# Performance work log

Measured on AMD Instinct MI355X. Metric: run time of the kernel, lower is better.

## Reference

```python
import jax, jax.numpy as jnp
import numpy as np

DIM = 1024
HEADS = 16
HEAD_DIM = 64
INNER = HEADS * HEAD_DIM  # 1024
SCALE = 8.0
LN_EPS = 1e-5
NORM_EPS = 1e-12  # F.normalize default eps


def layer_norm(x, g, b):
    m = jnp.mean(x, axis=-1, keepdims=True)
    v = jnp.mean((x - m) ** 2, axis=-1, keepdims=True)
    return (x - m) * jax.lax.rsqrt(v + LN_EPS) * g + b


def l2_normalize(x):
    n = jnp.sqrt(jnp.sum(x * x, axis=-1, keepdims=True))
    return x / jnp.maximum(n, NORM_EPS)


def setup_inputs() -> dict:
    key = jax.random.key(0)
    ks = jax.random.split(key, 8)
    B, N, T = 4, 4096, 256
    s = 0.02
    return {
        "x": jax.random.normal(ks[0], (B, N, DIM), jnp.float32),
        "context": jax.random.normal(ks[1], (B, T, DIM), jnp.float32),
        "Wq": jax.random.normal(ks[2], (DIM, INNER), jnp.float32) * s,
        "Wkv": jax.random.normal(ks[3], (DIM, 2 * INNER), jnp.float32) * s,
        "Wo": jax.random.normal(ks[4], (INNER, DIM), jnp.float32) * s,
        "null_kv": jax.random.normal(ks[5], (2, HEAD_DIM), jnp.float32),
        "q_scale": jnp.ones((HEAD_DIM,), jnp.float32),
        "k_scale": jnp.ones((HEAD_DIM,), jnp.float32),
        "ln_in_g": jnp.ones((DIM,), jnp.float32),
        "ln_in_b": jnp.zeros((DIM,), jnp.float32),
        "ln_ctx_g": jnp.ones((DIM,), jnp.float32),
        "ln_ctx_b": jnp.zeros((DIM,), jnp.float32),
        "ln_out_g": jnp.ones((DIM,), jnp.float32),
        "ln_out_b": jnp.zeros((DIM,), jnp.float32),
    }


def reference(x, context, Wq, Wkv, Wo, null_kv, q_scale, k_scale,
              ln_in_g, ln_in_b, ln_ctx_g, ln_ctx_b, ln_out_g, ln_out_b):
    B, N, _ = x.shape
    T = context.shape[1]
    xn = layer_norm(x, ln_in_g, ln_in_b)
    cn = layer_norm(context, ln_ctx_g, ln_ctx_b)
    q = xn @ Wq                      # [B, N, INNER]
    kv = cn @ Wkv                    # [B, T, 2*INNER]
    k, v = jnp.split(kv, 2, axis=-1)
    # split heads: b s (h d) -> b h s d
    def split_heads(t):
        b, s, _ = t.shape
        return t.reshape(b, s, HEADS, HEAD_DIM).transpose(0, 2, 1, 3)
    q, k, v = split_heads(q), split_heads(k), split_heads(v)
    # null kv token appended along kv-seq dim
    nk = jnp.broadcast_to(null_kv[0], (B, HEADS, 1, HEAD_DIM))
    nv = jnp.broadcast_to(null_kv[1], (B, HEADS, 1, HEAD_DIM))
    k = jnp.concatenate([k, nk], axis=2)   # [B, H, T+1, D]
    v = jnp.concatenate([v, nv], axis=2)
    q = l2_normalize(q) * q_scale
    k = l2_normalize(k) * k_scale
    scores = jnp.einsum('bhid,bhkd->bhik', q, k) * SCALE
    attn = jax.nn.softmax(scores, axis=-1)
    out = jnp.einsum('bhik,bhkd->bhid', attn, v)   # [B, H, N, D]
    out = out.transpose(0, 2, 1, 3).reshape(B, N, INNER)
    out = out @ Wo
    return layer_norm(out, ln_out_g, ln_out_b)
```

## Files before the change

kernel.cpp:

```cpp
#include <hip/hip_runtime.h>
#include <cstdint>
#include <cstddef>

typedef _Float16 f16;
typedef _Float16 f16x4 __attribute__((ext_vector_type(4)));
typedef _Float16 f16x8 __attribute__((ext_vector_type(8)));
typedef float f32x4 __attribute__((ext_vector_type(4)));

#define DIM 1024
#define B_ 4
#define N_ 4096
#define TKP 288
#define SCALE_ 8.0f
#define LOG2E 1.4426950408889634f

__device__ __forceinline__ void gload_lds16(const void* g, void* l) {
  __builtin_amdgcn_global_load_lds(
      reinterpret_cast<const __attribute__((address_space(1))) uint32_t*>(
          reinterpret_cast<uintptr_t>(g)),
      reinterpret_cast<__attribute__((address_space(3))) uint32_t*>(
          reinterpret_cast<uintptr_t>(l)),
      16, 0, 0);
}

__global__ void transpose_w_kernel(const float* __restrict__ W, f16* __restrict__ WT,
                                   int K, int N) {
  __shared__ float tile[32][33];
  int nt = N >> 5;
  int tk = blockIdx.x / nt, tn = blockIdx.x % nt;
  int tx = threadIdx.x & 31, ty = threadIdx.x >> 5;
#pragma unroll
  for (int p = 0; p < 32; p += 8)
    tile[ty + p][tx] = W[(size_t)(tk * 32 + ty + p) * N + tn * 32 + tx];
  __syncthreads();
#pragma unroll
  for (int p = 0; p < 32; p += 8)
    WT[(size_t)(tn * 32 + ty + p) * K + tk * 32 + tx] = (f16)tile[tx][ty + p];
}

template <typename OUT_T>
__global__ void ln_kernel(const float* __restrict__ in, const float* __restrict__ g,
                          const float* __restrict__ bb, OUT_T* __restrict__ out) {
  int row = blockIdx.x;
  int t = threadIdx.x;
  const float4* rp = (const float4*)(in + (size_t)row * DIM);
  float4 v = rp[t];
  float s = v.x + v.y + v.z + v.w;
  float ss = v.x * v.x + v.y * v.y + v.z * v.z + v.w * v.w;
#pragma unroll
  for (int m = 1; m < 64; m <<= 1) { s += __shfl_xor(s, m); ss += __shfl_xor(ss, m); }
  __shared__ float red[8];
  int w = t >> 6;
  if ((t & 63) == 0) { red[w * 2] = s; red[w * 2 + 1] = ss; }
  __syncthreads();
  s = red[0] + red[2] + red[4] + red[6];
  ss = red[1] + red[3] + red[5] + red[7];
  float mean = s * (1.0f / DIM);
  float var = ss * (1.0f / DIM) - mean * mean;
  float rstd = rsqrtf(var + 1e-5f);
  float4 gv = ((const float4*)g)[t];
  float4 bv = ((const float4*)bb)[t];
  float o0 = (v.x - mean) * rstd * gv.x + bv.x;
  float o1 = (v.y - mean) * rstd * gv.y + bv.y;
  float o2 = (v.z - mean) * rstd * gv.z + bv.z;
  float o3 = (v.w - mean) * rstd * gv.w + bv.w;
  if constexpr (sizeof(OUT_T) == 2) {
    f16x4 h = {(f16)o0, (f16)o1, (f16)o2, (f16)o3};
    *(f16x4*)((f16*)out + (size_t)row * DIM + t * 4) = h;
  } else {
    float4 o = {o0, o1, o2, o3};
    *(float4*)((float*)out + (size_t)row * DIM + t * 4) = o;
  }
}

template <bool OUT_F32>
__global__ __launch_bounds__(256, 2) void gemm_nt_kernel(
    const f16* __restrict__ A, const f16* __restrict__ Bt, void* __restrict__ C,
    int M, int N, int K) {
  __shared__ f16 As[128 * 64];
  __shared__ f16 Bs[128 * 64];
  int nb = N >> 7;
  int cpx = gridDim.x >> 3;
  int wg = ((int)blockIdx.x & 7) * cpx + ((int)blockIdx.x >> 3);
  int bm = wg / nb, bn = wg % nb;
  int t = threadIdx.x;
  int lane = t & 63, w = t >> 6;
  int wm = w >> 1, wn = w & 1;
  int r16 = lane & 15, g4 = lane >> 4;
  f32x4 acc[4][4] = {};
  for (int k0 = 0; k0 < K; k0 += 64) {
#pragma unroll
    for (int i = 0; i < 4; ++i) {
      int li = i * 256 + t;
      int r = li >> 3, c = li & 7;
      int kc = ((c ^ (r & 7)) << 3);
      gload_lds16(A + (size_t)(bm * 128 + r) * K + k0 + kc, (char*)As + li * 16);
      gload_lds16(Bt + (size_t)(bn * 128 + r) * K + k0 + kc, (char*)Bs + li * 16);
    }
    asm volatile("s_waitcnt vmcnt(0)" ::: "memory");
    __syncthreads();
#pragma unroll
    for (int ks = 0; ks < 2; ++ks) {
      f16x8 af[4], bf[4];
#pragma unroll
      for (int mi = 0; mi < 4; ++mi) {
        int r = wm * 64 + mi * 16 + r16;
        int cidx = ks * 4 + g4;
        af[mi] = *(const f16x8*)(As + r * 64 + ((cidx ^ (r & 7)) << 3));
      }
#pragma unroll
      for (int ni = 0; ni < 4; ++ni) {
        int r = wn * 64 + ni * 16 + r16;
        int cidx = ks * 4 + g4;
        bf[ni] = *(const f16x8*)(Bs + r * 64 + ((cidx ^ (r & 7)) << 3));
      }
#pragma unroll
      for (int mi = 0; mi < 4; ++mi)
#pragma unroll
        for (int ni = 0; ni < 4; ++ni)
          acc[mi][ni] = __builtin_amdgcn_mfma_f32_16x16x32_f16(af[mi], bf[ni],
                                                               acc[mi][ni], 0, 0, 0);
    }
    __syncthreads();
  }
  int cr0 = bm * 128 + wm * 64;
  int cc = bn * 128 + wn * 64 + r16;
#pragma unroll
  for (int mi = 0; mi < 4; ++mi)
#pragma unroll
    for (int ni = 0; ni < 4; ++ni)
#pragma unroll
      for (int j = 0; j < 4; ++j) {
        int row = cr0 + mi * 16 + g4 * 4 + j;
        int col = cc + ni * 16;
        if constexpr (OUT_F32)
          ((float*)C)[(size_t)row * N + col] = acc[mi][ni][j];
        else
          ((f16*)C)[(size_t)row * N + col] = (f16)acc[mi][ni][j];
      }
}

__global__ void prep_kv_kernel(const f16* __restrict__ kv, const float* __restrict__ nullkv,
                               const float* __restrict__ ks, f16* __restrict__ Karr,
                               f16* __restrict__ Varr) {
  int bh = blockIdx.x;
  int b = bh >> 4, h = bh & 15;
  int t = threadIdx.x;
  __shared__ f16 vt[256][65];
  const f16* krow = kv + (size_t)(b * 256 + t) * 2048 + h * 64;
  const f16* vrow = krow + 1024;
  f16x8 kd[8];
  float ss = 0.0f;
#pragma unroll
  for (int i = 0; i < 8; ++i) {
    kd[i] = *(const f16x8*)(krow + i * 8);
#pragma unroll
    for (int j = 0; j < 8; ++j) { float x = (float)kd[i][j]; ss += x * x; }
  }
  float inv = 1.0f / fmaxf(sqrtf(ss), 1e-12f);
  f16* kout = Karr + ((size_t)bh * TKP + t) * 64;
#pragma unroll
  for (int i = 0; i < 8; ++i) {
    f16x8 o;
#pragma unroll
    for (int j = 0; j < 8; ++j) o[j] = (f16)((float)kd[i][j] * inv * ks[i * 8 + j]);
    *(f16x8*)(kout + i * 8) = o;
  }
#pragma unroll
  for (int i = 0; i < 8; ++i) {
    f16x8 vv = *(const f16x8*)(vrow + i * 8);
#pragma unroll
    for (int j = 0; j < 8; ++j) vt[t][i * 8 + j] = vv[j];
  }
  if (t < 32) {
    f16* kr = Karr + ((size_t)bh * TKP + 256 + t) * 64;
    if (t == 0) {
      float ssn = 0.0f;
      for (int d = 0; d < 64; ++d) ssn += nullkv[d] * nullkv[d];
      float invn = 1.0f / fmaxf(sqrtf(ssn), 1e-12f);
      for (int d = 0; d < 64; ++d) kr[d] = (f16)(nullkv[d] * invn * ks[d]);
    } else {
      for (int d = 0; d < 64; ++d) kr[d] = (f16)0.0f;
    }
  }
  __syncthreads();
  f16* vbase = Varr + (size_t)bh * 64 * TKP;
  int pcol = (t & ~31) | (((t & 15) << 1) | ((t >> 4) & 1));
  for (int d = 0; d < 64; ++d) vbase[(size_t)d * TKP + pcol] = vt[t][d];
#pragma unroll
  for (int i = 0; i < 8; ++i) {
    int idx = i * 256 + t;
    int d = idx >> 5, key = 256 + (idx & 31);
    vbase[(size_t)d * TKP + key] = (key == 256) ? (f16)nullkv[64 + d] : (f16)0.0f;
  }
}

__global__ __launch_bounds__(256, 4) void attn_kernel(
    const f16* __restrict__ Q, const f16* __restrict__ Karr,
    const f16* __restrict__ Varr, const float* __restrict__ qs,
    const float* __restrict__ ksc, f16* __restrict__ O) {
  int wgid = ((int)blockIdx.x & 7) * 256 + ((int)blockIdx.x >> 3);
  int qb = wgid & 31, bh = wgid >> 5;
  int b = bh >> 4, h = bh & 15;
  int t = threadIdx.x, lane = t & 63, w = t >> 6;
  int r16 = lane & 15, g4 = lane >> 4;
  int row0 = b * N_ + qb * 128 + w * 32;
  int col0 = h * 64;
  const f16* Kp = Karr + (size_t)bh * TKP * 64;
  const f16* Vp = Varr + (size_t)bh * 64 * TKP;
  __shared__ f16 Plds[4][32 * 40];
  f16* Pw = &Plds[w][0];
  float mq = fabsf(qs[lane]), mk = fabsf(ksc[lane]);
#pragma unroll
  for (int m = 1; m < 64; m <<= 1) {
    mq = fmaxf(mq, __shfl_xor(mq, m));
    mk = fmaxf(mk, __shfl_xor(mk, m));
  }
  const float c1 = SCALE_ * LOG2E;
  const float c2 = SCALE_ * mq * mk * LOG2E;
  float qsv[2][8];
#pragma unroll
  for (int kdh = 0; kdh < 2; ++kdh)
#pragma unroll
    for (int i = 0; i < 8; ++i) qsv[kdh][i] = qs[kdh * 32 + g4 * 8 + i];
  f16x8 qf[2][2];
#pragma unroll
  for (int mi = 0; mi < 2; ++mi) {
    float f[2][8];
    float ssq = 0.0f;
#pragma unroll
    for (int kdh = 0; kdh < 2; ++kdh) {
      f16x8 v = *(const f16x8*)(Q + (size_t)(row0 + mi * 16 + r16) * DIM +
                                col0 + kdh * 32 + g4 * 8);
#pragma unroll
      for (int i = 0; i < 8; ++i) { f[kdh][i] = (float)v[i]; ssq += f[kdh][i] * f[kdh][i]; }
    }
    ssq += __shfl_xor(ssq, 16);
    ssq += __shfl_xor(ssq, 32);
    float inv = 1.0f / fmaxf(sqrtf(ssq), 1e-12f);
#pragma unroll
    for (int kdh = 0; kdh < 2; ++kdh) {
      f16x8 o;
#pragma unroll
      for (int i = 0; i < 8; ++i) o[i] = (f16)(f[kdh][i] * inv * qsv[kdh][i]);
      qf[mi][kdh] = o;
    }
  }
  f32x4 o[2][4] = {};
  float part[2][4] = {};
  for (int kt = 0; kt < 9; ++kt) {
    int key0 = kt * 32;
    f16x8 kf[2][2];
#pragma unroll
    for (int ni = 0; ni < 2; ++ni)
#pragma unroll
      for (int kdh = 0; kdh < 2; ++kdh)
        kf[ni][kdh] = *(const f16x8*)(Kp + (size_t)(key0 + ni * 16 + r16) * 64 +
                                      kdh * 32 + g4 * 8);
    f32x4 s[2][2] = {};
    __builtin_amdgcn_s_setprio(1);
#pragma unroll
    for (int kdh = 0; kdh < 2; ++kdh)
#pragma unroll
      for (int mi = 0; mi < 2; ++mi)
#pragma unroll
        for (int ni = 0; ni < 2; ++ni)
          s[mi][ni] = __builtin_amdgcn_mfma_f32_16x16x32_f16(qf[mi][kdh], kf[ni][kdh],
                                                             s[mi][ni], 0, 0, 0);
    __builtin_amdgcn_s_setprio(0);
    bool va = (key0 + r16 <= 256), vb = (key0 + 16 + r16 <= 256);
#pragma unroll
    for (int mi = 0; mi < 2; ++mi) {
#pragma unroll
      for (int j = 0; j < 4; ++j) {
        float p0 = exp2f(s[mi][0][j] * c1 - c2);
        float p1 = exp2f(s[mi][1][j] * c1 - c2);
        p0 = va ? p0 : 0.0f;
        p1 = vb ? p1 : 0.0f;
        part[mi][j] += p0 + p1;
        int prow = mi * 16 + g4 * 4 + j;
        auto pk = __builtin_amdgcn_cvt_pkrtz(p0, p1);
        ((uint32_t*)(Pw + prow * 40))[r16] = __builtin_bit_cast(uint32_t, pk);
      }
    }
    f16x8 vf[4];
#pragma unroll
    for (int nd = 0; nd < 4; ++nd)
      vf[nd] = *(const f16x8*)(Vp + (size_t)(nd * 16 + r16) * TKP + key0 + g4 * 8);
    __builtin_amdgcn_s_setprio(1);
#pragma unroll
    for (int mi = 0; mi < 2; ++mi) {
      f16x8 pa = *(const f16x8*)(Pw + (mi * 16 + r16) * 40 + g4 * 8);
#pragma unroll
      for (int nd = 0; nd < 4; ++nd)
        o[mi][nd] = __builtin_amdgcn_mfma_f32_16x16x32_f16(pa, vf[nd], o[mi][nd], 0, 0, 0);
    }
    __builtin_amdgcn_s_setprio(0);
  }
#pragma unroll
  for (int mi = 0; mi < 2; ++mi)
#pragma unroll
    for (int j = 0; j < 4; ++j) {
      float v = part[mi][j];
      v += __shfl_xor(v, 1); v += __shfl_xor(v, 2);
      v += __shfl_xor(v, 4); v += __shfl_xor(v, 8);
      part[mi][j] = v;
    }
#pragma unroll
  for (int mi = 0; mi < 2; ++mi)
#pragma unroll
    for (int j = 0; j < 4; ++j) {
      float inv = 1.0f / part[mi][j];
      int row = row0 + mi * 16 + g4 * 4 + j;
#pragma unroll
      for (int nd = 0; nd < 4; ++nd)
        O[(size_t)row * DIM + col0 + nd * 16 + r16] = (f16)(o[mi][nd][j] * inv);
    }
}

extern "C" void kernel_launch(void* const* d_in, const int* in_sizes, int n_in,
                              void* d_out, int out_size, void* d_ws, size_t ws_size,
                              hipStream_t stream) {
  const float* x      = (const float*)d_in[0];
  const float* ctx    = (const float*)d_in[1];
  const float* Wq     = (const float*)d_in[2];
  const float* Wkv    = (const float*)d_in[3];
  const float* Wo     = (const float*)d_in[4];
  const float* nullkv = (const float*)d_in[5];
  const float* qs     = (const float*)d_in[6];
  const float* ks     = (const float*)d_in[7];
  const float* g_in   = (const float*)d_in[8];
  const float* b_in   = (const float*)d_in[9];
  const float* g_ctx  = (const float*)d_in[10];
  const float* b_ctx  = (const float*)d_in[11];
  const float* g_out  = (const float*)d_in[12];
  const float* b_out  = (const float*)d_in[13];

  char* ws = (char*)d_ws;
  const size_t MB = 1ull << 20;
  f16* wqT   = (f16*)(ws + 0);
  f16* wkvT  = (f16*)(ws + 2 * MB);
  f16* woT   = (f16*)(ws + 6 * MB);
  f16* karr  = (f16*)(ws + 8 * MB);
  f16* varr  = (f16*)(ws + 11 * MB);
  f16* cn    = (f16*)(ws + 14 * MB);
  f16* kvb   = (f16*)(ws + 16 * MB);
  f16* xn    = (f16*)(ws + 20 * MB);
  f16* q_raw = (f16*)(ws + 52 * MB);
  f16* aout  = (f16*)(ws + 20 * MB);
  float* out2 = (float*)(ws + 52 * MB);

  transpose_w_kernel<<<1024, 256, 0, stream>>>(Wq, wqT, 1024, 1024);
  transpose_w_kernel<<<2048, 256, 0, stream>>>(Wkv, wkvT, 1024, 2048);
  transpose_w_kernel<<<1024, 256, 0, stream>>>(Wo, woT, 1024, 1024);

  ln_kernel<f16><<<16384, 256, 0, stream>>>(x, g_in, b_in, xn);
  ln_kernel<f16><<<1024, 256, 0, stream>>>(ctx, g_ctx, b_ctx, cn);

  gemm_nt_kernel<false><<<(16384 / 128) * (1024 / 128), 256, 0, stream>>>(
      xn, wqT, (void*)q_raw, 16384, 1024, 1024);
  gemm_nt_kernel<false><<<(1024 / 128) * (2048 / 128), 256, 0, stream>>>(
      cn, wkvT, (void*)kvb, 1024, 2048, 1024);

  prep_kv_kernel<<<64, 256, 0, stream>>>(kvb, nullkv, ks, karr, varr);

  attn_kernel<<<2048, 256, 0, stream>>>(q_raw, karr, varr, qs, ks, aout);

  gemm_nt_kernel<true><<<(16384 / 128) * (1024 / 128), 256, 0, stream>>>(
      aout, woT, (void*)out2, 16384, 1024, 1024);

  ln_kernel<float><<<16384, 256, 0, stream>>>(out2, g_out, b_out, (float*)d_out);
}
```

Before: 356.7 us.

## Store output projection in fp16, prefetch K tiles, and cheapen softmax in attention

The output projection GEMM now writes fp16 instead of fp32, and the final layer norm reads fp16. This halves the traffic of that intermediate round trip at some cost in precision before normalization. The attention loop now prefetches the next K tile and the V tile early, and replaces select-based masking with a large bias subtraction. It also uses the raw exp2 builtin and accumulates the row sums with fdot2 on the packed fp16 probabilities. These changes cut VALU work and hide load latency.

New measurement: 339.5 us. -4.8%, faster.

```diff
diff --git a/kernel.cpp b/kernel.cpp
--- a/kernel.cpp
+++ b/kernel.cpp
@@ -6,6 +6,7 @@
 typedef _Float16 f16x4 __attribute__((ext_vector_type(4)));
 typedef _Float16 f16x8 __attribute__((ext_vector_type(8)));
 typedef float f32x4 __attribute__((ext_vector_type(4)));
+typedef __fp16 h16x2 __attribute__((ext_vector_type(2)));
 
 #define DIM 1024
 #define B_ 4
@@ -38,13 +39,18 @@
     WT[(size_t)(tn * 32 + ty + p) * K + tk * 32 + tx] = (f16)tile[tx][ty + p];
 }
 
-template <typename OUT_T>
-__global__ void ln_kernel(const float* __restrict__ in, const float* __restrict__ g,
+template <typename IN_T, typename OUT_T>
+__global__ void ln_kernel(const IN_T* __restrict__ in, const float* __restrict__ g,
                           const float* __restrict__ bb, OUT_T* __restrict__ out) {
   int row = blockIdx.x;
   int t = threadIdx.x;
-  const float4* rp = (const float4*)(in + (size_t)row * DIM);
-  float4 v = rp[t];
+  float4 v;
+  if constexpr (sizeof(IN_T) == 2) {
+    f16x4 h = ((const f16x4*)((const f16*)in + (size_t)row * DIM))[t];
+    v = {(float)h[0], (float)h[1], (float)h[2], (float)h[3]};
+  } else {
+    v = ((const float4*)((const float*)in + (size_t)row * DIM))[t];
+  }
   float s = v.x + v.y + v.z + v.w;
   float ss = v.x * v.x + v.y * v.y + v.z * v.z + v.w * v.w;
 #pragma unroll
@@ -248,15 +254,22 @@
   }
   f32x4 o[2][4] = {};
   float part[2][4] = {};
+  const h16x2 ones2 = {(__fp16)1.0f, (__fp16)1.0f};
+  f16x8 kf[2][2];
+#pragma unroll
+  for (int ni = 0; ni < 2; ++ni)
+#pragma unroll
+    for (int kdh = 0; kdh < 2; ++kdh)
+      kf[ni][kdh] = *(const f16x8*)(Kp + (size_t)(ni * 16 + r16) * 64 +
+                                    kdh * 32 + g4 * 8);
   for (int kt = 0; kt < 9; ++kt) {
     int key0 = kt * 32;
-    f16x8 kf[2][2];
-#pragma unroll
-    for (int ni = 0; ni < 2; ++ni)
-#pragma unroll
-      for (int kdh = 0; kdh < 2; ++kdh)
-        kf[ni][kdh] = *(const f16x8*)(Kp + (size_t)(key0 + ni * 16 + r16) * 64 +
-                                      kdh * 32 + g4 * 8);
+    f16x8 vf[4];
+#pragma unroll
+    for (int nd = 0; nd < 4; ++nd)
+      vf[nd] = *(const f16x8*)(Vp + (size_t)(nd * 16 + r16) * TKP + key0 + g4 * 8);
+    float nb0 = (key0 + r16 <= 256) ? -c2 : -(c2 + 128.0f);
+    float nb1 = (key0 + 16 + r16 <= 256) ? -c2 : -(c2 + 128.0f);
     f32x4 s[2][2] = {};
     __builtin_amdgcn_s_setprio(1);
 #pragma unroll
@@ -268,25 +281,26 @@
           s[mi][ni] = __builtin_amdgcn_mfma_f32_16x16x32_f16(qf[mi][kdh], kf[ni][kdh],
                                                              s[mi][ni], 0, 0, 0);
     __builtin_amdgcn_s_setprio(0);
-    bool va = (key0 + r16 <= 256), vb = (key0 + 16 + r16 <= 256);
+    if (kt < 8) {
+#pragma unroll
+      for (int ni = 0; ni < 2; ++ni)
+#pragma unroll
+        for (int kdh = 0; kdh < 2; ++kdh)
+          kf[ni][kdh] = *(const f16x8*)(Kp + (size_t)(key0 + 32 + ni * 16 + r16) * 64 +
+                                        kdh * 32 + g4 * 8);
+    }
 #pragma unroll
     for (int mi = 0; mi < 2; ++mi) {
 #pragma unroll
       for (int j = 0; j < 4; ++j) {
-        float p0 = exp2f(s[mi][0][j] * c1 - c2);
-        float p1 = exp2f(s[mi][1][j] * c1 - c2);
-        p0 = va ? p0 : 0.0f;
-        p1 = vb ? p1 : 0.0f;
-        part[mi][j] += p0 + p1;
+        float p0 = __builtin_amdgcn_exp2f(s[mi][0][j] * c1 + nb0);
+        float p1 = __builtin_amdgcn_exp2f(s[mi][1][j] * c1 + nb1);
+        h16x2 pk = __builtin_amdgcn_cvt_pkrtz(p0, p1);
+        part[mi][j] = __builtin_amdgcn_fdot2(pk, ones2, part[mi][j], false);
         int prow = mi * 16 + g4 * 4 + j;
-        auto pk = __builtin_amdgcn_cvt_pkrtz(p0, p1);
         ((uint32_t*)(Pw + prow * 40))[r16] = __builtin_bit_cast(uint32_t, pk);
       }
     }
-    f16x8 vf[4];
-#pragma unroll
-    for (int nd = 0; nd < 4; ++nd)
-      vf[nd] = *(const f16x8*)(Vp + (size_t)(nd * 16 + r16) * TKP + key0 + g4 * 8);
     __builtin_amdgcn_s_setprio(1);
 #pragma unroll
     for (int mi = 0; mi < 2; ++mi) {
@@ -348,14 +362,14 @@
   f16* xn    = (f16*)(ws + 20 * MB);
   f16* q_raw = (f16*)(ws + 52 * MB);
   f16* aout  = (f16*)(ws + 20 * MB);
-  float* out2 = (float*)(ws + 52 * MB);
+  f16* out2h = (f16*)(ws + 52 * MB);
 
   transpose_w_kernel<<<1024, 256, 0, stream>>>(Wq, wqT, 1024, 1024);
   transpose_w_kernel<<<2048, 256, 0, stream>>>(Wkv, wkvT, 1024, 2048);
   transpose_w_kernel<<<1024, 256, 0, stream>>>(Wo, woT, 1024, 1024);
 
-  ln_kernel<f16><<<16384, 256, 0, stream>>>(x, g_in, b_in, xn);
-  ln_kernel<f16><<<1024, 256, 0, stream>>>(ctx, g_ctx, b_ctx, cn);
+  ln_kernel<float, f16><<<16384, 256, 0, stream>>>(x, g_in, b_in, xn);
+  ln_kernel<float, f16><<<1024, 256, 0, stream>>>(ctx, g_ctx, b_ctx, cn);
 
   gemm_nt_kernel<false><<<(16384 / 128) * (1024 / 128), 256, 0, stream>>>(
       xn, wqT, (void*)q_raw, 16384, 1024, 1024);
@@ -366,8 +380,8 @@
 
   attn_kernel<<<2048, 256, 0, stream>>>(q_raw, karr, varr, qs, ks, aout);
 
-  gemm_nt_kernel<true><<<(16384 / 128) * (1024 / 128), 256, 0, stream>>>(
-      aout, woT, (void*)out2, 16384, 1024, 1024);
-
-  ln_kernel<float><<<16384, 256, 0, stream>>>(out2, g_out, b_out, (float*)d_out);
-}
+  gemm_nt_kernel<false><<<(16384 / 128) * (1024 / 128), 256, 0, stream>>>(
+      aout, woT, (void*)out2h, 16384, 1024, 1024);
+
+  ln_kernel<f16, float><<<16384, 256, 0, stream>>>(out2h, g_out, b_out, (float*)d_out);
+}
```
